# Performance work log

Hardware: AMD Instinct MI355X
Metric: run time of the kernel (lower is better)

Reference implementation:

```python
import jax, jax.numpy as jnp
import numpy as np

IOU_THR = 0.5
NEG_POS = 3
CONF_W = 1.0
LOC_W = 1.0


def setup_inputs() -> dict:
    key = jax.random.key(0)
    ks = jax.random.split(key, 6)
    B, A, G = 16, 65536, 32
    ac = jax.random.uniform(ks[0], (B, A, 2))
    asz = jax.random.uniform(ks[1], (B, A, 2)) * 0.28 + 0.02
    anchors = jnp.concatenate([ac - asz / 2, ac + asz / 2], -1)
    gc = jax.random.uniform(ks[2], (B, G, 2))
    gsz = jax.random.uniform(ks[3], (B, G, 2)) * 0.28 + 0.02
    gt_boxes = jnp.concatenate([gc - gsz / 2, gc + gsz / 2], -1)
    bbox_pred = anchors + 0.05 * jax.random.normal(ks[4], (B, A, 4))
    # probabilities strictly inside (0,1) for BCE
    conf_pred = jax.random.uniform(ks[5], (B, A)) * 0.98 + 0.01
    return {"bbox_pred": bbox_pred, "conf_pred": conf_pred,
            "anchors": anchors, "gt_boxes": gt_boxes}


def _box_iou(a, g):
    # a: [A,4] xyxy, g: [G,4] xyxy -> [A,G]
    lt = jnp.maximum(a[:, None, :2], g[None, :, :2])
    rb = jnp.minimum(a[:, None, 2:], g[None, :, 2:])
    wh = jnp.clip(rb - lt, 0.0)
    inter = wh[..., 0] * wh[..., 1]
    area_a = (a[:, 2] - a[:, 0]) * (a[:, 3] - a[:, 1])
    area_g = (g[:, 2] - g[:, 0]) * (g[:, 3] - g[:, 1])
    return inter / (area_a[:, None] + area_g[None, :] - inter)


def _bce(p, t):
    return -(t * jnp.log(p) + (1.0 - t) * jnp.log1p(-p))


def _smooth_l1(x):
    ax = jnp.abs(x)
    return jnp.where(ax < 1.0, 0.5 * ax * ax, ax - 0.5)


def _per_image(bp, cp, an, gt):
    # bp: [A,4] pred boxes, cp: [A] conf, an: [A,4] anchors, gt: [G,4]
    A = cp.shape[0]
    ious = _box_iou(an, gt)                      # [A,G]
    best_gt_iou = ious.max(1)                    # [A]
    best_gt_idx = ious.argmax(1)                 # [A]
    best_anchor_idx = ious.argmax(0)             # [G] force-match each gt
    mask = (best_gt_iou > IOU_THR).at[best_anchor_idx].set(True)
    num_pos = mask.sum()

    # localization loss (center/size parameterization), summed over positives
    matched = gt[best_gt_idx]                    # [A,4]
    pc = (bp[:, :2] + bp[:, 2:]) / 2
    ps = bp[:, 2:] - bp[:, :2]
    gc = (matched[:, :2] + matched[:, 2:]) / 2
    gs = matched[:, 2:] - matched[:, :2]
    loc = _smooth_l1(jnp.concatenate([pc, ps], 1) - jnp.concatenate([gc, gs], 1)).sum(1)
    loc_loss = jnp.where(mask, loc, 0.0).sum()

    # confidence loss with hard negative mining
    t = mask.astype(cp.dtype)
    bce = _bce(cp, t)
    pos_loss = jnp.where(mask, bce, 0.0).sum()
    neg_bce = jnp.where(mask, 0.0, bce)
    num_neg = jnp.minimum(num_pos * NEG_POS, A - num_pos)
    sorted_neg = -jnp.sort(-neg_bce)             # descending
    neg_loss = jnp.where(jnp.arange(A) < num_neg, sorted_neg, 0.0).sum()
    conf_loss = pos_loss / jnp.maximum(num_pos, 1) + neg_loss / jnp.maximum(num_neg, 1)
    return loc_loss, conf_loss, num_pos


def reference(bbox_pred, conf_pred, anchors, gt_boxes):
    loc, conf, npos = jax.vmap(_per_image)(bbox_pred, conf_pred, anchors, gt_boxes)
    B = bbox_pred.shape[0]
    total_npos = jnp.maximum(npos.sum(), 1)
    total_loc = loc.sum() / total_npos * LOC_W
    total_conf = conf.sum() / B * CONF_W
    return total_loc + total_conf
```

## Files before the change

### kernel.cpp

```cpp
#include <hip/hip_runtime.h>

#define BB 16
#define AA 65536
#define GG 32
#define NB 8192
#define KOFF 59904u
#define AT 4
#define APB (256 * AT)
#define MBLK (AA / APB)
#define NSEG 64
#define SEGA (AA / NSEG)

__device__ unsigned char  g_mask[(size_t)BB * AA];
__device__ unsigned char  g_bidx[(size_t)BB * AA];
__device__ unsigned short g_nkey[(size_t)BB * NSEG * SEGA];
__device__ int   g_ncnt[BB * NSEG];
__device__ float g_spart[BB * NSEG * 2];
__device__ int   g_npart[BB * NSEG];
__device__ float g_loc[BB], g_pos[BB], g_neg[BB];
__device__ int   g_npos[BB], g_nneg[BB];

#define DYN_U32 (BB * GG * 2 + 2)
__device__ unsigned int g_dyn[DYN_U32];
__device__ __forceinline__ unsigned long long* fkeyp() {
    return (unsigned long long*)g_dyn;
}
__device__ __forceinline__ int* donep() {
    return (int*)(g_dyn + BB * GG * 2);
}

__device__ __forceinline__ float midval(int bin) {
    return __uint_as_float((((unsigned int)bin + KOFF) << 14) | 8192u);
}

__global__ void __launch_bounds__(256, 4)
k_matchforce(const float4* __restrict__ anchors,
             const float4* __restrict__ gts) {
    __shared__ float4 sg[GG];
    __shared__ unsigned long long wkey[4][GG];
    const int b = blockIdx.y;
    const int t = threadIdx.x;
    const int wave = t >> 6, lane = t & 63;
    if (t < GG) sg[t] = gts[(size_t)b * GG + t];
    __syncthreads();

    const size_t abase = (size_t)b * AA + (size_t)blockIdx.x * APB;

    float ax0[AT], ay0[AT], ax1[AT], ay1[AT], aar[AT], best[AT];
    int bg[AT];
#pragma unroll
    for (int j = 0; j < AT; ++j) {
        const float4 av = anchors[abase + j * 256 + t];
        ax0[j] = av.x; ay0[j] = av.y; ax1[j] = av.z; ay1[j] = av.w;
        aar[j] = (av.z - av.x) * (av.w - av.y);
        best[j] = -1.0f; bg[j] = 0;
    }

#pragma unroll 2
    for (int g = 0; g < GG; ++g) {
        const float4 gb = sg[g];
        const float ga = (gb.z - gb.x) * (gb.w - gb.y);
        float fbest = -1.0f;
        int fo = t;
#pragma unroll
        for (int j = 0; j < AT; ++j) {
            const float lx = fmaxf(ax0[j], gb.x), ly = fmaxf(ay0[j], gb.y);
            const float rx = fminf(ax1[j], gb.z), ry = fminf(ay1[j], gb.w);
            const float w = fmaxf(rx - lx, 0.0f), h = fmaxf(ry - ly, 0.0f);
            const float inter = w * h;
            const float s = aar[j] + ga;
            const float r = inter * __builtin_amdgcn_rcpf(s);
            if (r > best[j]) { best[j] = r; bg[j] = g; }
            if (r > fbest)   { fbest = r; fo = j * 256 + t; }
        }
        unsigned long long key =
            ((unsigned long long)__float_as_uint(fbest) << 32) |
            (unsigned long long)(0xFFFFFFFFu - (unsigned int)fo);
#pragma unroll
        for (int off = 1; off < 64; off <<= 1) {
            const unsigned long long o = __shfl_xor(key, off, 64);
            if (o > key) key = o;
        }
        if (lane == 0) wkey[wave][g] = key;
    }

#pragma unroll
    for (int j = 0; j < AT; ++j) {
        g_mask[abase + j * 256 + t] = (best[j] > (1.0f / 3.0f)) ? 1 : 0;
        g_bidx[abase + j * 256 + t] = (unsigned char)bg[j];
    }
    __syncthreads();
    if (t < GG) {
        unsigned long long k = wkey[0][t];
#pragma unroll
        for (int w = 1; w < 4; ++w) {
            const unsigned long long k1 = wkey[w][t];
            if (k1 > k) k = k1;
        }
        const unsigned int off = 0xFFFFFFFFu - (unsigned int)(k & 0xFFFFFFFFull);
        const unsigned int ga = (unsigned int)(blockIdx.x * APB) + off;
        atomicMax(&fkeyp()[b * GG + t],
                  (k & 0xFFFFFFFF00000000ull) |
                  (unsigned long long)(0xFFFFFFFFu - ga));
    }
}

__global__ void k_stats(const float4* __restrict__ bbox,
                        const float* __restrict__ conf,
                        const float4* __restrict__ gts) {
    __shared__ float4 sg[GG];
    __shared__ unsigned int bmap[SEGA / 32];
    __shared__ unsigned short nk[SEGA];
    __shared__ unsigned int ncnt;
    __shared__ float rf[256], rf2[256];
    __shared__ unsigned int ru[256];
    const int b = blockIdx.y, seg = blockIdx.x, t = threadIdx.x;
    if (t < GG) sg[t] = gts[(size_t)b * GG + t];
    if (t < SEGA / 32) bmap[t] = 0u;
    if (t == 0) ncnt = 0u;
    __syncthreads();
    if (t < GG) {
        const unsigned long long k = fkeyp()[b * GG + t];
        const unsigned int a = 0xFFFFFFFFu - (unsigned int)(k & 0xFFFFFFFFull);
        const int la = (int)a - seg * SEGA;
        if (la >= 0 && la < SEGA) atomicOr(&bmap[la >> 5], 1u << (la & 31));
    }
    __syncthreads();

    const size_t base = (size_t)b * AA + (size_t)seg * SEGA;
    const float4* c4 = (const float4*)(conf + base);
    const uchar4* m4 = (const uchar4*)(g_mask + base);
    const uchar4* x4 = (const uchar4*)(g_bidx + base);
    const float4* bb4 = bbox + base;

    float pos = 0.0f, loc = 0.0f;
    int np = 0;
    {
        const int idx = t;
        const float4 p4 = c4[idx];
        const uchar4 mm = m4[idx];
        const uchar4 xx = x4[idx];
        const unsigned int bw = (bmap[idx >> 3] >> ((idx & 7) * 4)) & 0xFu;
        const float pv[4] = {p4.x, p4.y, p4.z, p4.w};
        const unsigned char mv[4] = {mm.x, mm.y, mm.z, mm.w};
        const unsigned char xv[4] = {xx.x, xx.y, xx.z, xx.w};
        unsigned short lk[4];
        int ln = 0;
#pragma unroll
        for (int c = 0; c < 4; ++c) {
            const float p = pv[c];
            if (mv[c] | ((bw >> c) & 1u)) {
                np += 1;
                pos += -logf(p);
                const float4 bv = bb4[4 * idx + c];
                const float4 gb = sg[xv[c]];
                const float d0 = (bv.x + bv.z) * 0.5f - (gb.x + gb.z) * 0.5f;
                const float d1 = (bv.y + bv.w) * 0.5f - (gb.y + gb.w) * 0.5f;
                const float d2 = (bv.z - bv.x) - (gb.z - gb.x);
                const float d3 = (bv.w - bv.y) - (gb.w - gb.y);
                float ds[4] = {d0, d1, d2, d3};
#pragma unroll
                for (int q = 0; q < 4; ++q) {
                    float ax = fabsf(ds[q]);
                    loc += (ax < 1.0f) ? 0.5f * ax * ax : ax - 0.5f;
                }
            } else {
                const float nb = -log1pf(-p);
                int key = (int)(__float_as_uint(nb) >> 14) - (int)KOFF;
                key = key < 0 ? 0 : (key > NB - 1 ? NB - 1 : key);
                lk[ln++] = (unsigned short)key;
            }
        }
        if (ln) {
            const unsigned int slot = atomicAdd(&ncnt, (unsigned int)ln);
            for (int i = 0; i < ln; ++i) nk[slot + i] = lk[i];
        }
    }
    ru[t] = (unsigned int)np; rf[t] = pos; rf2[t] = loc;
    __syncthreads();
    if (t == 0 && (ncnt & 1u)) nk[ncnt] = 0xFFFFu;
    for (int w = 128; w > 0; w >>= 1) {
        if (t < w) { ru[t] += ru[t + w]; rf[t] += rf[t + w]; rf2[t] += rf2[t + w]; }
        __syncthreads();
    }
    if (t == 0) {
        g_npart[b * NSEG + seg] = (int)ru[0];
        g_spart[(b * NSEG + seg) * 2 + 0] = rf[0];
        g_spart[(b * NSEG + seg) * 2 + 1] = rf2[0];
        g_ncnt[b * NSEG + seg] = (int)ncnt;
    }
    const unsigned int cw = (ncnt + 1u) >> 1;
    const unsigned int* nk32 = (const unsigned int*)nk;
    unsigned int* outk = (unsigned int*)(g_nkey + ((size_t)b * NSEG + seg) * SEGA);
    for (unsigned int j = t; j < cw; j += 256) outk[j] = nk32[j];
}

__global__ void __launch_bounds__(1024) k_select(unsigned int* __restrict__ out) {
    __shared__ unsigned int hist[NB];
    __shared__ unsigned int ru[1024];
    __shared__ unsigned int s2[32];
    __shared__ int scw[NSEG];
    __shared__ float sh_pos, sh_loc;
    __shared__ int sh_np, sh_k, sh_bsel;
    __shared__ unsigned int sh_take;
    __shared__ float rf[1024];

    const int b = blockIdx.x, t = threadIdx.x;
    for (int j = t; j < NB; j += 1024) hist[j] = 0u;
    if (t < NSEG) scw[t] = (g_ncnt[b * NSEG + t] + 1) >> 1;
    if (t < 64) {
        int np = g_npart[b * NSEG + t];
        float pos = g_spart[(b * NSEG + t) * 2 + 0];
        float loc = g_spart[(b * NSEG + t) * 2 + 1];
#pragma unroll
        for (int off = 32; off > 0; off >>= 1) {
            np  += __shfl_xor(np,  off, 64);
            pos += __shfl_xor(pos, off, 64);
            loc += __shfl_xor(loc, off, 64);
        }
        if (t == 0) { sh_np = np; sh_pos = pos; sh_loc = loc; }
    }
    __syncthreads();
    {
        const unsigned int* kbase =
            (const unsigned int*)(g_nkey + (size_t)b * NSEG * SEGA);
#pragma unroll 4
        for (int w = t; w < NSEG * (SEGA / 2); w += 1024) {
            const int s = w >> 9;
            const int j = w & 511;
            if (j < scw[s]) {
                const unsigned int v = kbase[w];
                atomicAdd(&hist[v & 0xFFFFu], 1u);
                const unsigned int k1 = v >> 16;
                if (k1 != 0xFFFFu) atomicAdd(&hist[k1], 1u);
            }
        }
    }
    __syncthreads();
    const int np_tot = sh_np;

    unsigned int c = 0;
    const int hi = NB - 1 - t * 8;
#pragma unroll
    for (int j = 0; j < 8; ++j) c += hist[hi - j];
    ru[t] = c;
    __syncthreads();
    if (t < 32) {
        unsigned int x = 0;
#pragma unroll
        for (int j = 0; j < 32; ++j) x += ru[t * 32 + j];
        s2[t] = x;
    }
    __syncthreads();
    if (t == 0) {
        int k = 3 * np_tot;
        const int maxneg = AA - np_tot;
        if (k > maxneg) k = maxneg;
        sh_k = k;
        int bsel = NB;
        unsigned int take = 0;
        if (k > 0) {
            unsigned int cum = 0;
            int u = 0;
            while (u < 31 && cum + s2[u] < (unsigned int)k) { cum += s2[u]; ++u; }
            int cc = u * 32;
            while (cc < 1023 && cum + ru[cc] < (unsigned int)k) { cum += ru[cc]; ++cc; }
            const int h2 = NB - 1 - cc * 8;
            int j = 0;
            while (j < 7 && cum + hist[h2 - j] < (unsigned int)k) { cum += hist[h2 - j]; ++j; }
            bsel = h2 - j;
            take = (unsigned int)k - cum;
        }
        sh_bsel = bsel; sh_take = take;
    }
    __syncthreads();
    const int bsel = sh_bsel;
    float negp = 0.0f;
    for (int j = t; j < NB; j += 1024)
        if (j > bsel) { unsigned int cnt = hist[j]; if (cnt) negp += (float)cnt * midval(j); }
    rf[t] = negp;
    __syncthreads();
    for (int w = 512; w > 0; w >>= 1) {
        if (t < w) rf[t] += rf[t + w];
        __syncthreads();
    }
    if (t == 0) {
        float neg = 0.0f;
        if (sh_k > 0) neg = rf[0] + (float)sh_take * midval(bsel < NB ? bsel : 0);
        g_loc[b] = sh_loc; g_pos[b] = sh_pos; g_neg[b] = neg;
        g_npos[b] = np_tot; g_nneg[b] = sh_k;

        __threadfence();
        const int old = atomicAdd(donep(), 1);
        if (old == BB - 1) {
            __threadfence();
            float loc = 0.0f, conf = 0.0f;
            int tot = 0;
            for (int bb = 0; bb < BB; ++bb) {
                const float lv = __hip_atomic_load(&g_loc[bb],  __ATOMIC_RELAXED, __HIP_MEMORY_SCOPE_AGENT);
                const float pv = __hip_atomic_load(&g_pos[bb],  __ATOMIC_RELAXED, __HIP_MEMORY_SCOPE_AGENT);
                const float nv = __hip_atomic_load(&g_neg[bb],  __ATOMIC_RELAXED, __HIP_MEMORY_SCOPE_AGENT);
                const int   np = __hip_atomic_load(&g_npos[bb], __ATOMIC_RELAXED, __HIP_MEMORY_SCOPE_AGENT);
                const int   nn = __hip_atomic_load(&g_nneg[bb], __ATOMIC_RELAXED, __HIP_MEMORY_SCOPE_AGENT);
                loc += lv;
                conf += pv / (float)(np > 1 ? np : 1) +
                        nv / (float)(nn > 1 ? nn : 1);
                tot += np;
            }
            const float total = loc / (float)(tot > 1 ? tot : 1) + conf / (float)BB;
            const unsigned int u = __float_as_uint(total);
            const unsigned int r = 0x7FFFu + ((u >> 16) & 1u);
            const unsigned int bf = (u + r) >> 16;
            out[0] = (bf << 16) | bf;
        }
    }
}

extern "C" void kernel_launch(void* const* d_in, const int* in_sizes, int n_in,
                              void* d_out, int out_size, void* d_ws, size_t ws_size,
                              hipStream_t stream) {
    const float4* bbox    = (const float4*)d_in[0];
    const float*  conf    = (const float*)d_in[1];
    const float4* anchors = (const float4*)d_in[2];
    const float4* gts     = (const float4*)d_in[3];

    static unsigned int* dynp = nullptr;
    if (!dynp) hipGetSymbolAddress((void**)&dynp, HIP_SYMBOL(g_dyn));
    hipMemsetAsync(dynp, 0, sizeof(unsigned int) * DYN_U32, stream);

    k_matchforce<<<dim3(MBLK, BB), 256, 0, stream>>>(anchors, gts);
    k_stats<<<dim3(NSEG, BB), 256, 0, stream>>>(bbox, conf, gts);
    k_select<<<BB, 1024, 0, stream>>>((unsigned int*)d_out);
}
```

Measured before the change: 141.6 us.

## Fuse stats and select kernels via last-block pattern and drop memset

The per-segment stats kernel and the per-image select kernel become one kernel. The last segment block of each image, found with an atomic counter, does the histogram selection, so one launch goes away. The force-match atomicMax into a memset buffer is replaced by per-block partial keys that each consumer reduces with wave shuffles, which removes the hipMemsetAsync. The counters are reset inside the first kernel instead. Segments grow to 16 per image with 1024 threads each, which cuts parallelism and adds a serial tail in the last block.

```diff
diff --git a/kernel.cpp b/kernel.cpp
--- a/kernel.cpp
+++ b/kernel.cpp
@@ -8,26 +8,20 @@
 #define AT 4
 #define APB (256 * AT)
 #define MBLK (AA / APB)
-#define NSEG 64
+#define NSEG 16
 #define SEGA (AA / NSEG)
 
 __device__ unsigned char  g_mask[(size_t)BB * AA];
 __device__ unsigned char  g_bidx[(size_t)BB * AA];
+__device__ unsigned long long g_fpart[(size_t)BB * GG * MBLK];
 __device__ unsigned short g_nkey[(size_t)BB * NSEG * SEGA];
 __device__ int   g_ncnt[BB * NSEG];
 __device__ float g_spart[BB * NSEG * 2];
 __device__ int   g_npart[BB * NSEG];
 __device__ float g_loc[BB], g_pos[BB], g_neg[BB];
 __device__ int   g_npos[BB], g_nneg[BB];
-
-#define DYN_U32 (BB * GG * 2 + 2)
-__device__ unsigned int g_dyn[DYN_U32];
-__device__ __forceinline__ unsigned long long* fkeyp() {
-    return (unsigned long long*)g_dyn;
-}
-__device__ __forceinline__ int* donep() {
-    return (int*)(g_dyn + BB * GG * 2);
-}
+__device__ int   g_sdone[BB];
+__device__ int   g_done;
 
 __device__ __forceinline__ float midval(int bin) {
     return __uint_as_float((((unsigned int)bin + KOFF) << 14) | 8192u);
@@ -41,6 +35,10 @@
     const int b = blockIdx.y;
     const int t = threadIdx.x;
     const int wave = t >> 6, lane = t & 63;
+    if (blockIdx.x == 0 && b == 0) {
+        if (t < BB) g_sdone[t] = 0;
+        else if (t == BB) g_done = 0;
+    }
     if (t < GG) sg[t] = gts[(size_t)b * GG + t];
     __syncthreads();
 
@@ -99,31 +97,52 @@
         }
         const unsigned int off = 0xFFFFFFFFu - (unsigned int)(k & 0xFFFFFFFFull);
         const unsigned int ga = (unsigned int)(blockIdx.x * APB) + off;
-        atomicMax(&fkeyp()[b * GG + t],
-                  (k & 0xFFFFFFFF00000000ull) |
-                  (unsigned long long)(0xFFFFFFFFu - ga));
+        g_fpart[((size_t)b * GG + t) * MBLK + blockIdx.x] =
+            (k & 0xFFFFFFFF00000000ull) |
+            (unsigned long long)(0xFFFFFFFFu - ga);
     }
 }
 
-__global__ void k_stats(const float4* __restrict__ bbox,
-                        const float* __restrict__ conf,
-                        const float4* __restrict__ gts) {
+__global__ void __launch_bounds__(1024)
+k_fused(const float4* __restrict__ bbox,
+        const float* __restrict__ conf,
+        const float4* __restrict__ gts,
+        unsigned int* __restrict__ out) {
     __shared__ float4 sg[GG];
     __shared__ unsigned int bmap[SEGA / 32];
     __shared__ unsigned short nk[SEGA];
     __shared__ unsigned int ncnt;
-    __shared__ float rf[256], rf2[256];
-    __shared__ unsigned int ru[256];
+    __shared__ float rf[1024], rf2[1024];
+    __shared__ unsigned int ru[1024];
+    __shared__ unsigned int hist[NB];
+    __shared__ unsigned int s2[32];
+    __shared__ int scw[NSEG];
+    __shared__ int sh_np, sh_k, sh_bsel, sh_last;
+    __shared__ float sh_pos, sh_loc;
+    __shared__ unsigned int sh_take;
+
     const int b = blockIdx.y, seg = blockIdx.x, t = threadIdx.x;
     if (t < GG) sg[t] = gts[(size_t)b * GG + t];
     if (t < SEGA / 32) bmap[t] = 0u;
     if (t == 0) ncnt = 0u;
     __syncthreads();
-    if (t < GG) {
-        const unsigned long long k = fkeyp()[b * GG + t];
-        const unsigned int a = 0xFFFFFFFFu - (unsigned int)(k & 0xFFFFFFFFull);
-        const int la = (int)a - seg * SEGA;
-        if (la >= 0 && la < SEGA) atomicOr(&bmap[la >> 5], 1u << (la & 31));
+
+    {
+        const int gg = t >> 5, p = t & 31;
+        const unsigned long long* fp =
+            &g_fpart[((size_t)b * GG + gg) * MBLK + p * 2];
+        unsigned long long k = fp[0];
+        { const unsigned long long v = fp[1]; if (v > k) k = v; }
+#pragma unroll
+        for (int off = 1; off < 32; off <<= 1) {
+            const unsigned long long o = __shfl_xor(k, off, 32);
+            if (o > k) k = o;
+        }
+        if (p == 0) {
+            const unsigned int a = 0xFFFFFFFFu - (unsigned int)(k & 0xFFFFFFFFull);
+            const int la = (int)a - seg * SEGA;
+            if (la >= 0 && la < SEGA) atomicOr(&bmap[la >> 5], 1u << (la & 31));
+        }
     }
     __syncthreads();
 
@@ -179,7 +198,7 @@
     ru[t] = (unsigned int)np; rf[t] = pos; rf2[t] = loc;
     __syncthreads();
     if (t == 0 && (ncnt & 1u)) nk[ncnt] = 0xFFFFu;
-    for (int w = 128; w > 0; w >>= 1) {
+    for (int w = 512; w > 0; w >>= 1) {
         if (t < w) { ru[t] += ru[t + w]; rf[t] += rf[t + w]; rf2[t] += rf2[t + w]; }
         __syncthreads();
     }
@@ -189,45 +208,44 @@
         g_spart[(b * NSEG + seg) * 2 + 1] = rf2[0];
         g_ncnt[b * NSEG + seg] = (int)ncnt;
     }
-    const unsigned int cw = (ncnt + 1u) >> 1;
-    const unsigned int* nk32 = (const unsigned int*)nk;
-    unsigned int* outk = (unsigned int*)(g_nkey + ((size_t)b * NSEG + seg) * SEGA);
-    for (unsigned int j = t; j < cw; j += 256) outk[j] = nk32[j];
-}
-
-__global__ void __launch_bounds__(1024) k_select(unsigned int* __restrict__ out) {
-    __shared__ unsigned int hist[NB];
-    __shared__ unsigned int ru[1024];
-    __shared__ unsigned int s2[32];
-    __shared__ int scw[NSEG];
-    __shared__ float sh_pos, sh_loc;
-    __shared__ int sh_np, sh_k, sh_bsel;
-    __shared__ unsigned int sh_take;
-    __shared__ float rf[1024];
-
-    const int b = blockIdx.x, t = threadIdx.x;
+    {
+        const unsigned int cw = (ncnt + 1u) >> 1;
+        const unsigned int* nk32 = (const unsigned int*)nk;
+        unsigned int* outk =
+            (unsigned int*)(g_nkey + ((size_t)b * NSEG + seg) * SEGA);
+        for (unsigned int j = t; j < cw; j += 1024) outk[j] = nk32[j];
+    }
+
+    __threadfence();
+    if (t == 0) {
+        const int old = atomicAdd(&g_sdone[b], 1);
+        sh_last = (old == NSEG - 1);
+    }
+    __syncthreads();
+    if (!sh_last) return;
+    __threadfence();
+
     for (int j = t; j < NB; j += 1024) hist[j] = 0u;
     if (t < NSEG) scw[t] = (g_ncnt[b * NSEG + t] + 1) >> 1;
-    if (t < 64) {
-        int np = g_npart[b * NSEG + t];
-        float pos = g_spart[(b * NSEG + t) * 2 + 0];
-        float loc = g_spart[(b * NSEG + t) * 2 + 1];
-#pragma unroll
-        for (int off = 32; off > 0; off >>= 1) {
-            np  += __shfl_xor(np,  off, 64);
-            pos += __shfl_xor(pos, off, 64);
-            loc += __shfl_xor(loc, off, 64);
-        }
-        if (t == 0) { sh_np = np; sh_pos = pos; sh_loc = loc; }
+    if (t < NSEG) {
+        int np2 = g_npart[b * NSEG + t];
+        float pos2 = g_spart[(b * NSEG + t) * 2 + 0];
+        float loc2 = g_spart[(b * NSEG + t) * 2 + 1];
+#pragma unroll
+        for (int off = 8; off > 0; off >>= 1) {
+            np2  += __shfl_xor(np2,  off, 16);
+            pos2 += __shfl_xor(pos2, off, 16);
+            loc2 += __shfl_xor(loc2, off, 16);
+        }
+        if (t == 0) { sh_np = np2; sh_pos = pos2; sh_loc = loc2; }
     }
     __syncthreads();
     {
         const unsigned int* kbase =
             (const unsigned int*)(g_nkey + (size_t)b * NSEG * SEGA);
-#pragma unroll 4
         for (int w = t; w < NSEG * (SEGA / 2); w += 1024) {
-            const int s = w >> 9;
-            const int j = w & 511;
+            const int s = w >> 11;
+            const int j = w & 2047;
             if (j < scw[s]) {
                 const unsigned int v = kbase[w];
                 atomicAdd(&hist[v & 0xFFFFu], 1u);
@@ -291,23 +309,23 @@
         g_npos[b] = np_tot; g_nneg[b] = sh_k;
 
         __threadfence();
-        const int old = atomicAdd(donep(), 1);
+        const int old = atomicAdd(&g_done, 1);
         if (old == BB - 1) {
             __threadfence();
-            float loc = 0.0f, conf = 0.0f;
+            float loc = 0.0f, conf2 = 0.0f;
             int tot = 0;
             for (int bb = 0; bb < BB; ++bb) {
                 const float lv = __hip_atomic_load(&g_loc[bb],  __ATOMIC_RELAXED, __HIP_MEMORY_SCOPE_AGENT);
                 const float pv = __hip_atomic_load(&g_pos[bb],  __ATOMIC_RELAXED, __HIP_MEMORY_SCOPE_AGENT);
                 const float nv = __hip_atomic_load(&g_neg[bb],  __ATOMIC_RELAXED, __HIP_MEMORY_SCOPE_AGENT);
-                const int   np = __hip_atomic_load(&g_npos[bb], __ATOMIC_RELAXED, __HIP_MEMORY_SCOPE_AGENT);
+                const int   np2 = __hip_atomic_load(&g_npos[bb], __ATOMIC_RELAXED, __HIP_MEMORY_SCOPE_AGENT);
                 const int   nn = __hip_atomic_load(&g_nneg[bb], __ATOMIC_RELAXED, __HIP_MEMORY_SCOPE_AGENT);
                 loc += lv;
-                conf += pv / (float)(np > 1 ? np : 1) +
-                        nv / (float)(nn > 1 ? nn : 1);
-                tot += np;
+                conf2 += pv / (float)(np2 > 1 ? np2 : 1) +
+                         nv / (float)(nn > 1 ? nn : 1);
+                tot += np2;
             }
-            const float total = loc / (float)(tot > 1 ? tot : 1) + conf / (float)BB;
+            const float total = loc / (float)(tot > 1 ? tot : 1) + conf2 / (float)BB;
             const unsigned int u = __float_as_uint(total);
             const unsigned int r = 0x7FFFu + ((u >> 16) & 1u);
             const unsigned int bf = (u + r) >> 16;
@@ -324,11 +342,7 @@
     const float4* anchors = (const float4*)d_in[2];
     const float4* gts     = (const float4*)d_in[3];
 
-    static unsigned int* dynp = nullptr;
-    if (!dynp) hipGetSymbolAddress((void**)&dynp, HIP_SYMBOL(g_dyn));
-    hipMemsetAsync(dynp, 0, sizeof(unsigned int) * DYN_U32, stream);
-
     k_matchforce<<<dim3(MBLK, BB), 256, 0, stream>>>(anchors, gts);
-    k_stats<<<dim3(NSEG, BB), 256, 0, stream>>>(bbox, conf, gts);
-    k_select<<<BB, 1024, 0, stream>>>((unsigned int*)d_out);
+    k_fused<<<dim3(NSEG, BB), 1024, 0, stream>>>(bbox, conf, gts,
+                                                 (unsigned int*)d_out);
 }
```

Result: slower. 233.1 us (+64.6%).
